# Optimization experiments

Measured on AMD Instinct MI355X. Metric: run time of the kernel, lower is better.

## Reference

```python
import jax, jax.numpy as jnp
import numpy as np

S = 160                 # image size (renderer default is 256; reduced for working-set budget)
SIGMA = 1.0             # soft-silhouette sharpness, in pixels
EPS = 1e-8
CHUNK = 512             # faces per rasterization chunk
ANGLE = np.pi / 2.0
VIEW_TAN = float(np.tan(np.radians(30.0)))   # nr.Renderer default viewing_angle=30
CAM_POS = np.array([0.0, 0.0, 2.732], dtype=np.float32)

# constant rotation: Rodrigues formula for axis-angle (pi/2 about y), as in nr.rotation_from_axis
_aa = ANGLE * np.array([0.0, 1.0, 0.0])
_th = np.linalg.norm(_aa)
_k = _aa / _th
_K = np.array([[0, -_k[2], _k[1]], [_k[2], 0, -_k[0]], [-_k[1], _k[0], 0]])
ROT = (np.eye(3) + np.sin(_th) * _K + (1 - np.cos(_th)) * (_K @ _K)).astype(np.float32)


def _make_uv_sphere(stacks=32, slices=64):
    verts = [[0.0, 0.0, 1.0]]
    for i in range(1, stacks):
        phi = np.pi * i / stacks
        for j in range(slices):
            th = 2 * np.pi * j / slices
            verts.append([np.sin(phi) * np.cos(th), np.sin(phi) * np.sin(th), np.cos(phi)])
    verts.append([0.0, 0.0, -1.0])
    V = len(verts)
    faces = []
    for j in range(slices):
        faces.append([0, 1 + j, 1 + (j + 1) % slices])
    for i in range(stacks - 2):
        r0 = 1 + i * slices
        r1 = r0 + slices
        for j in range(slices):
            a, b = r0 + j, r0 + (j + 1) % slices
            c, d = r1 + j, r1 + (j + 1) % slices
            faces.append([a, b, c])
            faces.append([b, d, c])
    r0 = 1 + (stacks - 2) * slices
    for j in range(slices):
        faces.append([V - 1, r0 + (j + 1) % slices, r0 + j])
    return np.asarray(verts, np.float32), np.asarray(faces, np.int32)


def setup_inputs() -> dict:
    key = jax.random.key(0)
    v, f = _make_uv_sphere()                     # V=1986, F=3968
    pad = 4096 - f.shape[0]
    f = np.concatenate([f, np.zeros((pad, 3), np.int32)], axis=0)  # degenerate pad faces
    image_ref = jax.random.uniform(key, (1, S, S), dtype=jnp.float32)
    return {"vertices": jnp.asarray(v)[None], "faces": jnp.asarray(f)[None], "image_ref": image_ref}


def _project(v):
    # world -> camera (rotate, place camera at z=2.732) -> perspective -> pixel coords
    vc = v @ ROT.T + CAM_POS                     # [V,3]
    xy = vc[:, :2] / (vc[:, 2:3] * VIEW_TAN)     # NDC in [-1,1]
    return (xy + 1.0) * (S / 2.0)                # [V,2] pixels


def _soft_coverage(pts, fv):
    # pts [P,2] pixel centers, fv [C,3,2] screen-space triangles -> coverage [P,C]
    a, b, c = fv[:, 0], fv[:, 1], fv[:, 2]

    def edge_dist(p0, p1):
        d = p1 - p0                                              # [C,2]
        cr = d[:, 0] * (pts[:, None, 1] - p0[None, :, 1]) - d[:, 1] * (pts[:, None, 0] - p0[None, :, 0])
        return cr / (jnp.sqrt(jnp.sum(d * d, -1)) + EPS)         # signed pixel distance [P,C]

    area = (b[:, 0] - a[:, 0]) * (c[:, 1] - a[:, 1]) - (b[:, 1] - a[:, 1]) * (c[:, 0] - a[:, 0])
    sg = jnp.where(area >= 0, 1.0, -1.0)[None, :]                # winding correction
    dmin = jnp.minimum(jnp.minimum(edge_dist(a, b) * sg, edge_dist(b, c) * sg), edge_dist(c, a) * sg)
    cov = jax.nn.sigmoid(dmin / SIGMA)
    return cov * (jnp.abs(area) > 1e-6)[None, :]                 # mask degenerate (padded) faces


def reference(vertices, faces, image_ref):
    v2 = _project(vertices[0])                   # [V,2]
    fv = v2[faces[0]]                            # [F,3,2]
    fvc = fv.reshape(-1, CHUNK, 3, 2)            # [F/CHUNK, CHUNK, 3, 2]
    ys, xs = jnp.meshgrid(jnp.arange(S, dtype=jnp.float32) + 0.5,
                          jnp.arange(S, dtype=jnp.float32) + 0.5, indexing="ij")
    pts = jnp.stack([xs.ravel(), ys.ravel()], -1)  # [P,2]

    cov_fn = jax.checkpoint(_soft_coverage)

    def body(not_cov, fvk):
        cov = cov_fn(pts, fvk)                   # [P,CHUNK]
        return not_cov * jnp.prod(1.0 - cov, axis=1), None

    not_cov, _ = jax.lax.scan(body, jnp.ones((S * S,), jnp.float32), fvc)
    images = (1.0 - not_cov).reshape(1, S, S)    # silhouette in [0,1]
    loss = jnp.sum((images - image_ref) ** 2)    # broadcast matches images - image_ref[None] in torch
    return images, loss
```

## Files before the change

### kernel.cpp

```cpp
#include <hip/hip_runtime.h>
#include <math.h>

#define S_IMG 160
#define NPIX (S_IMG * S_IMG)
#define NF 4096
#define TS 16
#define NTX 10
#define NTILE 100
#define CAP NF
#define MAXK 64
#define INV_LN2 1.4426950408889634f
#define CULL_THRESH -25.0f

#define ROT_EPS 6.123234e-17f
#define CAM_Z 2.732f
#define VIEW_TAN 0.5773502691896258f

#if __has_builtin(__builtin_amdgcn_exp2f)
#define EXP2F(x) __builtin_amdgcn_exp2f(x)
#else
#define EXP2F(x) exp2f(x)
#endif

__device__ __forceinline__ float2 project_vert(const float* __restrict__ v, int i) {
    float x = v[3 * i], y = v[3 * i + 1], z = v[3 * i + 2];
    float vx = fmaf(ROT_EPS, x, z);
    float vy = y;
    float vz = fmaf(ROT_EPS, z, -x) + CAM_Z;
    float denom = vz * VIEW_TAN;
    return make_float2((vx / denom + 1.0f) * (S_IMG * 0.5f),
                       (vy / denom + 1.0f) * (S_IMG * 0.5f));
}

__global__ void __launch_bounds__(512) setup_cull(const float* __restrict__ verts,
                                                  const int* __restrict__ faces,
                                                  float* __restrict__ list,
                                                  int* __restrict__ nk_arr) {
    const int t = blockIdx.x;
    const int tid = threadIdx.x;
    const int wid = tid >> 6;
    const int lane = tid & 63;
    const float cx = (float)((t % NTX) * TS) + 8.0f;
    const float cy = (float)((t / NTX) * TS) + 8.0f;

    __shared__ int wcnt[8];
    float* mylist = list + (size_t)t * CAP * 12;
    int base = 0;

    for (int r = 0; r < NF / 512; ++r) {
        int f = r * 512 + tid;
        int i0 = faces[3 * f], i1 = faces[3 * f + 1], i2 = faces[3 * f + 2];
        float2 a = project_vert(verts, i0);
        float2 b = project_vert(verts, i1);
        float2 c = project_vert(verts, i2);
        float area = (b.x - a.x) * (c.y - a.y) - (b.y - a.y) * (c.x - a.x);
        float sg = (area >= 0.0f) ? 1.0f : -1.0f;
        bool valid = fabsf(area) > 1e-6f;

        float o[9];
        float umin = 1e30f;
        float2 p0s[3] = {a, b, c};
        float2 p1s[3] = {b, c, a};
#pragma unroll
        for (int e = 0; e < 3; ++e) {
            float dx = p1s[e].x - p0s[e].x;
            float dy = p1s[e].y - p0s[e].y;
            float L = sqrtf(dx * dx + dy * dy) + 1e-8f;
            float s = sg * INV_LN2 / L;
            float A = valid ? (-dy * s) : 0.0f;
            float B = valid ? (dx * s) : 0.0f;
            float C = valid ? ((dy * p0s[e].x - dx * p0s[e].y) * s) : -1e30f;
            o[3 * e + 0] = A;
            o[3 * e + 1] = B;
            o[3 * e + 2] = C;
            float Cadj = valid ? fmaf(fabsf(A) + fabsf(B), 7.5f, C) : -1e30f;
            umin = fminf(umin, fmaf(A, cx, fmaf(B, cy, Cadj)));
        }
        bool pred = umin >= CULL_THRESH;
        unsigned long long m = __ballot(pred);
        int wpop = __popcll(m);
        int prefix = __popcll(m & ((1ull << lane) - 1ull));

        __syncthreads();
        if (lane == 0) wcnt[wid] = wpop;
        __syncthreads();
        int off = base;
#pragma unroll
        for (int w = 0; w < 8; ++w) {
            int cw = wcnt[w];
            if (w < wid) off += cw;
            base += cw;
        }
        off += prefix;
        if (pred) {
            float4* dst = (float4*)(mylist + (size_t)off * 12);
            dst[0] = make_float4(o[0], o[1], o[2], o[3]);
            dst[1] = make_float4(o[4], o[5], o[6], o[7]);
            dst[2] = make_float4(o[8], 0.0f, 0.0f, 0.0f);
        }
    }
    __syncthreads();

    int cnt = base;
    int nkt = (cnt + 63) >> 6;
    int padcnt = nkt * 64 - cnt;
    for (int i = tid; i < padcnt; i += 512) {
        float4* dst = (float4*)(mylist + (size_t)(cnt + i) * 12);
        dst[0] = make_float4(0.0f, 0.0f, -1e30f, 0.0f);
        dst[1] = make_float4(0.0f, -1e30f, 0.0f, 0.0f);
        dst[2] = make_float4(-1e30f, 0.0f, 0.0f, 0.0f);
    }
    if (tid == 0) nk_arr[t] = nkt;
}

__global__ void __launch_bounds__(64) cover(const float* __restrict__ list,
                                            const int* __restrict__ nk_arr,
                                            float* __restrict__ partials) {
    const int t = blockIdx.x;
    const int k = blockIdx.y;
    if (k >= nk_arr[t]) return;

    __shared__ float4 lds[64 * 3];
    const int lane = threadIdx.x;
    {
        const float4* src = (const float4*)(list + ((size_t)t * CAP + (size_t)k * 64) * 12);
#pragma unroll
        for (int i = 0; i < 3; ++i) lds[lane + i * 64] = src[lane + i * 64];
    }
    asm volatile("s_waitcnt lgkmcnt(0)" ::: "memory");

    const int colL = lane & 15;
    const int rowL = (lane >> 4) * 4;
    const float px = (float)((t % NTX) * TS + colL) + 0.5f;
    const float py0 = (float)((t / NTX) * TS + rowL) + 0.5f;
    const float py1 = py0 + 1.0f, py2 = py0 + 2.0f, py3 = py0 + 3.0f;

    float P0 = 1.0f, P1 = 1.0f, P2 = 1.0f, P3 = 1.0f;
    for (int j = 0; j < 64; ++j) {
        float4 c0 = lds[j];
        float4 c1 = lds[j + 64];
        float4 c2 = lds[j + 128];
        c0 = lds[3 * j];
        c1 = lds[3 * j + 1];
        c2 = lds[3 * j + 2];
        float b1 = fmaf(c0.x, px, c0.z);
        float b2 = fmaf(c0.w, px, c1.y);
        float b3 = fmaf(c1.z, px, c2.x);
        {
            float d1 = fmaf(c0.y, py0, b1), d2 = fmaf(c1.x, py0, b2), d3 = fmaf(c1.w, py0, b3);
            float e = EXP2F(fminf(fminf(d1, d2), d3));
            P0 = fmaf(P0, e, P0);
        }
        {
            float d1 = fmaf(c0.y, py1, b1), d2 = fmaf(c1.x, py1, b2), d3 = fmaf(c1.w, py1, b3);
            float e = EXP2F(fminf(fminf(d1, d2), d3));
            P1 = fmaf(P1, e, P1);
        }
        {
            float d1 = fmaf(c0.y, py2, b1), d2 = fmaf(c1.x, py2, b2), d3 = fmaf(c1.w, py2, b3);
            float e = EXP2F(fminf(fminf(d1, d2), d3));
            P2 = fmaf(P2, e, P2);
        }
        {
            float d1 = fmaf(c0.y, py3, b1), d2 = fmaf(c1.x, py3, b2), d3 = fmaf(c1.w, py3, b3);
            float e = EXP2F(fminf(fminf(d1, d2), d3));
            P3 = fmaf(P3, e, P3);
        }
    }

    size_t base = ((size_t)t * MAXK + k) * 256 + (size_t)rowL * 16 + colL;
    partials[base] = __builtin_amdgcn_rcpf(P0);
    partials[base + 16] = __builtin_amdgcn_rcpf(P1);
    partials[base + 32] = __builtin_amdgcn_rcpf(P2);
    partials[base + 48] = __builtin_amdgcn_rcpf(P3);
}

__global__ void __launch_bounds__(256) finish(const float* __restrict__ partials,
                                              const int* __restrict__ nk_arr,
                                              const float* __restrict__ img_ref,
                                              float* __restrict__ out,
                                              float* __restrict__ bsums) {
    const int t = blockIdx.x;
    const int tid = threadIdx.x;
    const int nkt = nk_arr[t];
    float prod = 1.0f;
    for (int k = 0; k < nkt; ++k) prod *= partials[((size_t)t * MAXK + k) * 256 + tid];
    float img = 1.0f - prod;
    int col = (t % NTX) * TS + (tid & 15);
    int row = (t / NTX) * TS + (tid >> 4);
    int p = row * S_IMG + col;
    out[p] = img;
    float d = img - img_ref[p];
    float sq = d * d;
#pragma unroll
    for (int off = 32; off > 0; off >>= 1) sq += __shfl_down(sq, off);
    __shared__ float red[4];
    int lane = tid & 63;
    int wid = tid >> 6;
    if (lane == 0) red[wid] = sq;
    __syncthreads();
    if (tid == 0) bsums[t] = (red[0] + red[1]) + (red[2] + red[3]);
}

__global__ void __launch_bounds__(64) loss_kernel(const float* __restrict__ bsums,
                                                  float* __restrict__ loss_out) {
    int lane = threadIdx.x;
    float v = 0.0f;
    if (lane < NTILE) v = bsums[lane];
    if (lane + 64 < NTILE) v += bsums[lane + 64];
#pragma unroll
    for (int off = 32; off > 0; off >>= 1) v += __shfl_down(v, off);
    if (lane == 0) loss_out[0] = v;
}

extern "C" void kernel_launch(void* const* d_in, const int* in_sizes, int n_in,
                              void* d_out, int out_size, void* d_ws, size_t ws_size,
                              hipStream_t stream) {
    const float* verts = (const float*)d_in[0];
    const int* faces = (const int*)d_in[1];
    const float* img_ref = (const float*)d_in[2];
    float* out = (float*)d_out;

    float* list = (float*)d_ws;
    float* partials = list + (size_t)NTILE * CAP * 12;
    int* nk_arr = (int*)(partials + (size_t)NTILE * MAXK * 256);
    float* bsums = (float*)(nk_arr + 128);

    setup_cull<<<NTILE, 512, 0, stream>>>(verts, faces, list, nk_arr);
    cover<<<dim3(NTILE, MAXK), 64, 0, stream>>>(list, nk_arr, partials);
    finish<<<NTILE, 256, 0, stream>>>(partials, nk_arr, img_ref, out, bsums);
    loss_kernel<<<1, 64, 0, stream>>>(bsums, out + NPIX);
}
```

Before: 38.05 us.

## Fuse cull, coverage and finish into one per-tile kernel with LDS-projected vertices

Merges the setup/cull, coverage and finish kernels into a single 512-thread block per tile. Vertices are projected once into shared memory instead of three times per face. The 8 waves of each block split the face chunks and reduce their partial products through LDS rather than a global partials buffer, which removes two launches and the global round-trip. The trade-off is lower parallelism: 100 blocks of 8 waves replace up to 6400 single-wave blocks, so a tile with many faces becomes a serial hotspot. It also swaps in rsq and rcp intrinsics, which are slightly less precise than the sqrt and divide they replace.

```diff
diff --git a/kernel.cpp b/kernel.cpp
--- a/kernel.cpp
+++ b/kernel.cpp
@@ -4,11 +4,11 @@
 #define S_IMG 160
 #define NPIX (S_IMG * S_IMG)
 #define NF 4096
+#define NV 1986
 #define TS 16
 #define NTX 10
 #define NTILE 100
 #define CAP NF
-#define MAXK 64
 #define INV_LN2 1.4426950408889634f
 #define CULL_THRESH -25.0f
 
@@ -22,39 +22,46 @@
 #define EXP2F(x) exp2f(x)
 #endif
 
-__device__ __forceinline__ float2 project_vert(const float* __restrict__ v, int i) {
-    float x = v[3 * i], y = v[3 * i + 1], z = v[3 * i + 2];
-    float vx = fmaf(ROT_EPS, x, z);
-    float vy = y;
-    float vz = fmaf(ROT_EPS, z, -x) + CAM_Z;
-    float denom = vz * VIEW_TAN;
-    return make_float2((vx / denom + 1.0f) * (S_IMG * 0.5f),
-                       (vy / denom + 1.0f) * (S_IMG * 0.5f));
-}
-
-__global__ void __launch_bounds__(512) setup_cull(const float* __restrict__ verts,
-                                                  const int* __restrict__ faces,
-                                                  float* __restrict__ list,
-                                                  int* __restrict__ nk_arr) {
+__global__ void __launch_bounds__(512) mega(const float* __restrict__ verts,
+                                            const int* __restrict__ faces,
+                                            float* __restrict__ list,
+                                            const float* __restrict__ img_ref,
+                                            float* __restrict__ out,
+                                            float* __restrict__ bsums) {
+    __shared__ float2 sverts[NV];
+    __shared__ float4 stage[8][64 * 3];
+    __shared__ float pacc[8][256];
+    __shared__ float red[8];
+    __shared__ int wcnt[8];
+
     const int t = blockIdx.x;
     const int tid = threadIdx.x;
     const int wid = tid >> 6;
     const int lane = tid & 63;
+
+    for (int i = tid; i < NV; i += 512) {
+        float x = verts[3 * i], y = verts[3 * i + 1], z = verts[3 * i + 2];
+        float vx = fmaf(ROT_EPS, x, z);
+        float vz = fmaf(ROT_EPS, z, -x) + CAM_Z;
+        float inv = __builtin_amdgcn_rcpf(vz * VIEW_TAN);
+        sverts[i] = make_float2(fmaf(vx * inv, 80.0f, 80.0f),
+                                fmaf(y * inv, 80.0f, 80.0f));
+    }
+    __syncthreads();
+
     const float cx = (float)((t % NTX) * TS) + 8.0f;
     const float cy = (float)((t / NTX) * TS) + 8.0f;
-
-    __shared__ int wcnt[8];
     float* mylist = list + (size_t)t * CAP * 12;
     int base = 0;
 
     for (int r = 0; r < NF / 512; ++r) {
         int f = r * 512 + tid;
         int i0 = faces[3 * f], i1 = faces[3 * f + 1], i2 = faces[3 * f + 2];
-        float2 a = project_vert(verts, i0);
-        float2 b = project_vert(verts, i1);
-        float2 c = project_vert(verts, i2);
+        float2 a = sverts[i0];
+        float2 b = sverts[i1];
+        float2 c = sverts[i2];
         float area = (b.x - a.x) * (c.y - a.y) - (b.y - a.y) * (c.x - a.x);
-        float sg = (area >= 0.0f) ? 1.0f : -1.0f;
+        float sg = (area >= 0.0f) ? INV_LN2 : -INV_LN2;
         bool valid = fabsf(area) > 1e-6f;
 
         float o[9];
@@ -65,16 +72,16 @@
         for (int e = 0; e < 3; ++e) {
             float dx = p1s[e].x - p0s[e].x;
             float dy = p1s[e].y - p0s[e].y;
-            float L = sqrtf(dx * dx + dy * dy) + 1e-8f;
-            float s = sg * INV_LN2 / L;
+            float dd = fmaf(dx, dx, dy * dy);
+            float s = sg * __builtin_amdgcn_rsqf(dd);
             float A = valid ? (-dy * s) : 0.0f;
             float B = valid ? (dx * s) : 0.0f;
             float C = valid ? ((dy * p0s[e].x - dx * p0s[e].y) * s) : -1e30f;
             o[3 * e + 0] = A;
             o[3 * e + 1] = B;
             o[3 * e + 2] = C;
-            float Cadj = valid ? fmaf(fabsf(A) + fabsf(B), 7.5f, C) : -1e30f;
-            umin = fminf(umin, fmaf(A, cx, fmaf(B, cy, Cadj)));
+            float bound = fmaf(fabsf(A) + fabsf(B), 7.5f, fmaf(A, cx, fmaf(B, cy, C)));
+            umin = fminf(umin, valid ? bound : -1e30f);
         }
         bool pred = umin >= CULL_THRESH;
         unsigned long long m = __ballot(pred);
@@ -101,33 +108,18 @@
     }
     __syncthreads();
 
-    int cnt = base;
-    int nkt = (cnt + 63) >> 6;
-    int padcnt = nkt * 64 - cnt;
-    for (int i = tid; i < padcnt; i += 512) {
-        float4* dst = (float4*)(mylist + (size_t)(cnt + i) * 12);
-        dst[0] = make_float4(0.0f, 0.0f, -1e30f, 0.0f);
-        dst[1] = make_float4(0.0f, -1e30f, 0.0f, 0.0f);
-        dst[2] = make_float4(-1e30f, 0.0f, 0.0f, 0.0f);
-    }
-    if (tid == 0) nk_arr[t] = nkt;
-}
-
-__global__ void __launch_bounds__(64) cover(const float* __restrict__ list,
-                                            const int* __restrict__ nk_arr,
-                                            float* __restrict__ partials) {
-    const int t = blockIdx.x;
-    const int k = blockIdx.y;
-    if (k >= nk_arr[t]) return;
-
-    __shared__ float4 lds[64 * 3];
-    const int lane = threadIdx.x;
+    const int cnt = base;
+    const int nkt = (cnt + 63) >> 6;
     {
-        const float4* src = (const float4*)(list + ((size_t)t * CAP + (size_t)k * 64) * 12);
-#pragma unroll
-        for (int i = 0; i < 3; ++i) lds[lane + i * 64] = src[lane + i * 64];
-    }
-    asm volatile("s_waitcnt lgkmcnt(0)" ::: "memory");
+        int padcnt = nkt * 64 - cnt;
+        for (int i = tid; i < padcnt; i += 512) {
+            float4* dst = (float4*)(mylist + (size_t)(cnt + i) * 12);
+            dst[0] = make_float4(0.0f, 0.0f, -64.0f, 0.0f);
+            dst[1] = make_float4(0.0f, -64.0f, 0.0f, 0.0f);
+            dst[2] = make_float4(-64.0f, 0.0f, 0.0f, 0.0f);
+        }
+    }
+    __syncthreads();
 
     const int colL = lane & 15;
     const int rowL = (lane >> 4) * 4;
@@ -136,70 +128,73 @@
     const float py1 = py0 + 1.0f, py2 = py0 + 2.0f, py3 = py0 + 3.0f;
 
     float P0 = 1.0f, P1 = 1.0f, P2 = 1.0f, P3 = 1.0f;
-    for (int j = 0; j < 64; ++j) {
-        float4 c0 = lds[j];
-        float4 c1 = lds[j + 64];
-        float4 c2 = lds[j + 128];
-        c0 = lds[3 * j];
-        c1 = lds[3 * j + 1];
-        c2 = lds[3 * j + 2];
-        float b1 = fmaf(c0.x, px, c0.z);
-        float b2 = fmaf(c0.w, px, c1.y);
-        float b3 = fmaf(c1.z, px, c2.x);
-        {
-            float d1 = fmaf(c0.y, py0, b1), d2 = fmaf(c1.x, py0, b2), d3 = fmaf(c1.w, py0, b3);
-            float e = EXP2F(fminf(fminf(d1, d2), d3));
-            P0 = fmaf(P0, e, P0);
-        }
-        {
-            float d1 = fmaf(c0.y, py1, b1), d2 = fmaf(c1.x, py1, b2), d3 = fmaf(c1.w, py1, b3);
-            float e = EXP2F(fminf(fminf(d1, d2), d3));
-            P1 = fmaf(P1, e, P1);
-        }
-        {
-            float d1 = fmaf(c0.y, py2, b1), d2 = fmaf(c1.x, py2, b2), d3 = fmaf(c1.w, py2, b3);
-            float e = EXP2F(fminf(fminf(d1, d2), d3));
-            P2 = fmaf(P2, e, P2);
-        }
-        {
-            float d1 = fmaf(c0.y, py3, b1), d2 = fmaf(c1.x, py3, b2), d3 = fmaf(c1.w, py3, b3);
-            float e = EXP2F(fminf(fminf(d1, d2), d3));
-            P3 = fmaf(P3, e, P3);
-        }
-    }
-
-    size_t base = ((size_t)t * MAXK + k) * 256 + (size_t)rowL * 16 + colL;
-    partials[base] = __builtin_amdgcn_rcpf(P0);
-    partials[base + 16] = __builtin_amdgcn_rcpf(P1);
-    partials[base + 32] = __builtin_amdgcn_rcpf(P2);
-    partials[base + 48] = __builtin_amdgcn_rcpf(P3);
-}
-
-__global__ void __launch_bounds__(256) finish(const float* __restrict__ partials,
-                                              const int* __restrict__ nk_arr,
-                                              const float* __restrict__ img_ref,
-                                              float* __restrict__ out,
-                                              float* __restrict__ bsums) {
-    const int t = blockIdx.x;
-    const int tid = threadIdx.x;
-    const int nkt = nk_arr[t];
-    float prod = 1.0f;
-    for (int k = 0; k < nkt; ++k) prod *= partials[((size_t)t * MAXK + k) * 256 + tid];
-    float img = 1.0f - prod;
-    int col = (t % NTX) * TS + (tid & 15);
-    int row = (t / NTX) * TS + (tid >> 4);
-    int p = row * S_IMG + col;
-    out[p] = img;
-    float d = img - img_ref[p];
-    float sq = d * d;
+    float4* myslot = stage[wid];
+
+    for (int k = wid; k < nkt; k += 8) {
+        const float4* src = (const float4*)(mylist + (size_t)k * 64 * 12);
+#pragma unroll
+        for (int i = 0; i < 3; ++i) myslot[lane + i * 64] = src[lane + i * 64];
+        asm volatile("s_waitcnt lgkmcnt(0)" ::: "memory");
+
+        for (int j = 0; j < 64; ++j) {
+            float4 c0 = myslot[3 * j];
+            float4 c1 = myslot[3 * j + 1];
+            float4 c2 = myslot[3 * j + 2];
+            float b1 = fmaf(c0.x, px, c0.z);
+            float b2 = fmaf(c0.w, px, c1.y);
+            float b3 = fmaf(c1.z, px, c2.x);
+            {
+                float d1 = fmaf(c0.y, py0, b1), d2 = fmaf(c1.x, py0, b2), d3 = fmaf(c1.w, py0, b3);
+                float e = EXP2F(fminf(fminf(d1, d2), d3));
+                P0 = fmaf(P0, e, P0);
+            }
+            {
+                float d1 = fmaf(c0.y, py1, b1), d2 = fmaf(c1.x, py1, b2), d3 = fmaf(c1.w, py1, b3);
+                float e = EXP2F(fminf(fminf(d1, d2), d3));
+                P1 = fmaf(P1, e, P1);
+            }
+            {
+                float d1 = fmaf(c0.y, py2, b1), d2 = fmaf(c1.x, py2, b2), d3 = fmaf(c1.w, py2, b3);
+                float e = EXP2F(fminf(fminf(d1, d2), d3));
+                P2 = fmaf(P2, e, P2);
+            }
+            {
+                float d1 = fmaf(c0.y, py3, b1), d2 = fmaf(c1.x, py3, b2), d3 = fmaf(c1.w, py3, b3);
+                float e = EXP2F(fminf(fminf(d1, d2), d3));
+                P3 = fmaf(P3, e, P3);
+            }
+        }
+        asm volatile("" ::: "memory");
+    }
+
+    pacc[wid][rowL * 16 + colL] = __builtin_amdgcn_rcpf(P0);
+    pacc[wid][(rowL + 1) * 16 + colL] = __builtin_amdgcn_rcpf(P1);
+    pacc[wid][(rowL + 2) * 16 + colL] = __builtin_amdgcn_rcpf(P2);
+    pacc[wid][(rowL + 3) * 16 + colL] = __builtin_amdgcn_rcpf(P3);
+    __syncthreads();
+
+    float sq = 0.0f;
+    if (tid < 256) {
+        float prod = 1.0f;
+#pragma unroll
+        for (int w = 0; w < 8; ++w) prod *= pacc[w][tid];
+        float img = 1.0f - prod;
+        int col = (t % NTX) * TS + (tid & 15);
+        int row = (t / NTX) * TS + (tid >> 4);
+        int p = row * S_IMG + col;
+        out[p] = img;
+        float d = img - img_ref[p];
+        sq = d * d;
+    }
 #pragma unroll
     for (int off = 32; off > 0; off >>= 1) sq += __shfl_down(sq, off);
-    __shared__ float red[4];
-    int lane = tid & 63;
-    int wid = tid >> 6;
     if (lane == 0) red[wid] = sq;
     __syncthreads();
-    if (tid == 0) bsums[t] = (red[0] + red[1]) + (red[2] + red[3]);
+    if (tid == 0) {
+        float s = ((red[0] + red[1]) + (red[2] + red[3])) +
+                  ((red[4] + red[5]) + (red[6] + red[7]));
+        bsums[t] = s;
+    }
 }
 
 __global__ void __launch_bounds__(64) loss_kernel(const float* __restrict__ bsums,
@@ -222,12 +217,8 @@
     float* out = (float*)d_out;
 
     float* list = (float*)d_ws;
-    float* partials = list + (size_t)NTILE * CAP * 12;
-    int* nk_arr = (int*)(partials + (size_t)NTILE * MAXK * 256);
-    float* bsums = (float*)(nk_arr + 128);
-
-    setup_cull<<<NTILE, 512, 0, stream>>>(verts, faces, list, nk_arr);
-    cover<<<dim3(NTILE, MAXK), 64, 0, stream>>>(list, nk_arr, partials);
-    finish<<<NTILE, 256, 0, stream>>>(partials, nk_arr, img_ref, out, bsums);
+    float* bsums = list + (size_t)NTILE * CAP * 12;
+
+    mega<<<NTILE, 512, 0, stream>>>(verts, faces, list, img_ref, out, bsums);
     loss_kernel<<<1, 64, 0, stream>>>(bsums, out + NPIX);
 }
```

Result: slower. 39.17 us (+3.0%).
